# Performance work log

Measured on AMD Instinct MI355X. Metric: run time of the kernel, lower is better.

Reference implementation:

```python
import jax, jax.numpy as jnp
import numpy as np

U = 512  # units

def hard_sigmoid(x):
    # Keras hard_sigmoid: clip(0.2*x + 0.5, 0, 1)
    return jnp.clip(0.2 * x + 0.5, 0.0, 1.0)

def setup_inputs() -> dict:
    key = jax.random.key(0)
    ks = jax.random.split(key, 9)
    B, T, A, D = 64, 2048, 512, 512  # batch, annotation steps, annotation units, input dim
    s = lambda k, shape, scale: jax.random.normal(k, shape, jnp.float32) * scale
    return {
        "inputs": s(ks[0], (B, D), 1.0),
        "h": s(ks[1], (B, U), 1.0),
        "c": s(ks[2], (B, U), 1.0),
        "annotations": s(ks[3], (B, T, A), 1.0),
        "kernel": s(ks[4], (D + A, 4 * U), 0.02),
        "recurrent_kernel": s(ks[5], (U, 4 * U), 0.02),
        "bias": jnp.zeros((6 * U,), jnp.float32).at[U:2 * U].set(1.0),  # unit_forget_bias
        "kernel_u": s(ks[6], (A, U), 0.02),
        "kernel_w": s(ks[7], (U, U), 0.02),
        "kernel_v": s(ks[8], (U,), 0.02),
    }

def reference(inputs, h, c, annotations, kernel, recurrent_kernel, bias, kernel_u, kernel_w, kernel_v):
    bias_u = bias[4 * U:5 * U]
    # precomputed annotation projection (done once in build()): [B,T,U]
    uh = jnp.einsum('bta,au->btu', annotations, kernel_u) + bias_u
    # Bahdanau attention scores
    Wxstm = h @ kernel_w                                   # [B,U]
    et = jnp.einsum('btu,u->bt', jnp.tanh(uh + Wxstm[:, None, :]), kernel_v)
    at = jax.nn.softmax(et, axis=1)                        # exp/sum in source == softmax
    context = jnp.einsum('bt,bta->ba', at, annotations)    # [B,A]
    x = jnp.concatenate([inputs, context], axis=-1)        # [B, D+A]
    z = x @ kernel + h @ recurrent_kernel + bias[:4 * U]   # [B,4U]
    i = hard_sigmoid(z[:, :U])
    f = hard_sigmoid(z[:, U:2 * U])
    c_new = f * c + i * jnp.tanh(z[:, 2 * U:3 * U])
    o = hard_sigmoid(z[:, 3 * U:])
    h_new = o * jnp.tanh(c_new)
    return h_new
```

## Files before the change

### kernel.cpp

```cpp
#include <hip/hip_runtime.h>

constexpr int U = 512;
constexpr int B = 64;
constexpr int T = 2048;
constexpr int A = 512;

typedef __attribute__((ext_vector_type(8))) short short8;
typedef __attribute__((ext_vector_type(4))) float f32x4;

__device__ __forceinline__ unsigned short f32_to_bf16(float f) {
    unsigned int b = __float_as_uint(f);
    unsigned int r = (b + 0x7FFFu + ((b >> 16) & 1u)) >> 16;
    return (unsigned short)r;
}

__device__ __forceinline__ float fast_tanh(float x) {
    float e = exp2f(x * 2.885390081777927f);
    return (e - 1.0f) * __builtin_amdgcn_rcpf(e + 1.0f);
}

__device__ __forceinline__ float hard_sigmoid(float z) {
    return fminf(fmaxf(0.2f * z + 0.5f, 0.0f), 1.0f);
}

__global__ __launch_bounds__(256) void k_prep_s(const float* __restrict__ h,
                                                const float* __restrict__ kw,
                                                float* __restrict__ Sp) {
    int b = blockIdx.x >> 2;
    int kc = blockIdx.x & 3;
    int u = threadIdx.x;
    const float* hb = h + b * U + kc * 128;
    const float* kwb = kw + (size_t)kc * 128 * U;
    float a0 = 0.f, a1 = 0.f;
#pragma unroll 4
    for (int k = 0; k < 128; ++k) {
        float hv = hb[k];
        a0 += hv * kwb[(size_t)k * U + u];
        a1 += hv * kwb[(size_t)k * U + u + 256];
    }
    float* p = Sp + ((size_t)kc * 64 + b) * U;
    p[u] = a0;
    p[u + 256] = a1;
}

__global__ __launch_bounds__(256) void k_s_reduce(const float* __restrict__ Sp,
                                                  const float* __restrict__ bias,
                                                  float* __restrict__ S) {
    int gid = blockIdx.x * 256 + threadIdx.x;
    int b = gid >> 9, u = gid & 511;
    float s = bias[4 * U + u];
#pragma unroll
    for (int kc = 0; kc < 4; ++kc) s += Sp[((size_t)kc * 64 + b) * U + u];
    S[gid] = s;
}

__global__ __launch_bounds__(256) void k_prep_kpack(const float* __restrict__ ku,
                                                    unsigned short* __restrict__ kpack) {
    int t = blockIdx.x >> 3;
    int gid = (blockIdx.x & 7) * 256 + threadIdx.x;
    int d = gid >> 9;
    int u = gid & 511;
    float vals[8];
#pragma unroll
    for (int e = 0; e < 8; ++e) vals[e] = ku[(size_t)(t * 32 + d * 8 + e) * U + u];
    int sc = d ^ ((u >> 1) & 3);
    short8 pk;
#pragma unroll
    for (int e = 0; e < 8; ++e) pk[e] = (short)f32_to_bf16(vals[e]);
    *(short8*)&kpack[(size_t)t * 16384 + u * 32 + sc * 8] = pk;
}

__global__ __launch_bounds__(256) void k_prep_wt(const float* __restrict__ kern,
                                                 const float* __restrict__ rk,
                                                 unsigned short* __restrict__ Wt) {
    __shared__ float tile[32][33];
    int k0 = blockIdx.x << 5;
    int j0 = blockIdx.y << 5;
    int c = threadIdx.x & 31, r0 = threadIdx.x >> 5;
#pragma unroll
    for (int p = 0; p < 4; ++p) {
        int r = r0 + p * 8;
        int k = k0 + r;
        float val = (k < 1024) ? kern[k * 2048 + j0 + c]
                               : rk[(k - 1024) * 2048 + j0 + c];
        tile[r][c] = val;
    }
    __syncthreads();
#pragma unroll
    for (int p = 0; p < 4; ++p) {
        int r = r0 + p * 8;
        Wt[(size_t)(j0 + r) * 1536 + k0 + c] = f32_to_bf16(tile[c][r]);
    }
}

__global__ __launch_bounds__(256, 2) void k_gemm_et(const float* __restrict__ ann,
                                                    const unsigned short* __restrict__ kpack,
                                                    const float* __restrict__ S,
                                                    const float* __restrict__ v,
                                                    float* __restrict__ mz,
                                                    float* __restrict__ part) {
    __shared__ unsigned short As[2][64 * 32];
    __shared__ unsigned short Bs[2][512 * 32];
    __shared__ float red[4][64];
    __shared__ float p_lds[64];

    const int tid = threadIdx.x;
    const int wave = tid >> 6;
    const int lane = tid & 63;
    const int lanelo = lane & 15;
    const int quad = lane >> 4;
    const int wn = wave;

    const int mt = blockIdx.x;
    const int b = mt >> 5;
    const float* aBase = ann + (size_t)mt * 64 * A;
    const char* kpB = (const char*)kpack;

    f32x4 acc[4][8];
#pragma unroll
    for (int i = 0; i < 4; ++i)
#pragma unroll
        for (int j = 0; j < 8; ++j) acc[i][j] = {0.f, 0.f, 0.f, 0.f};

    const int rowA = tid >> 2;
    const int c8A = tid & 3;
    f32x4 pv0, pv1;

    auto stage_b = [&](int t, int buf) {
        const char* src = kpB + (size_t)t * 32768;
#pragma unroll
        for (int p = 0; p < 8; ++p) {
            int seg = p * 4 + wave;
            __builtin_amdgcn_global_load_lds(
                (const __attribute__((address_space(1))) void*)(src + seg * 1024 + lane * 16),
                (__attribute__((address_space(3))) void*)((char*)&Bs[buf][0] + seg * 1024),
                16, 0, 0);
        }
    };

    auto cvt_store = [&](int buf) {
        short8 pk;
        pk[0] = (short)f32_to_bf16(pv0.x);
        pk[1] = (short)f32_to_bf16(pv0.y);
        pk[2] = (short)f32_to_bf16(pv0.z);
        pk[3] = (short)f32_to_bf16(pv0.w);
        pk[4] = (short)f32_to_bf16(pv1.x);
        pk[5] = (short)f32_to_bf16(pv1.y);
        pk[6] = (short)f32_to_bf16(pv1.z);
        pk[7] = (short)f32_to_bf16(pv1.w);
        *(short8*)&As[buf][rowA * 32 + ((c8A ^ ((rowA >> 1) & 3)) * 8)] = pk;
    };

    {
        const float* src = aBase + (size_t)rowA * A + c8A * 8;
        pv0 = *(const f32x4*)src;
        pv1 = *(const f32x4*)(src + 4);
    }
    stage_b(0, 0);
    cvt_store(0);
    __syncthreads();

    for (int t = 0; t < 16; ++t) {
        const int cur = t & 1;
        const int nxt = cur ^ 1;
        const bool more = (t < 15);

        if (more) {
            const float* src = aBase + (size_t)rowA * A + (t + 1) * 32 + c8A * 8;
            pv0 = *(const f32x4*)src;
            pv1 = *(const f32x4*)(src + 4);
            stage_b(t + 1, nxt);
        }

        short8 af[4];
#pragma unroll
        for (int mi = 0; mi < 4; ++mi) {
            int row = mi * 16 + lanelo;
            af[mi] = *(const short8*)&As[cur][row * 32 + ((quad ^ ((row >> 1) & 3)) * 8)];
        }
        short8 bfr[8];
#pragma unroll
        for (int ni = 0; ni < 8; ++ni) {
            int rowb = wn * 128 + ni * 16 + lanelo;
            bfr[ni] = *(const short8*)&Bs[cur][rowb * 32 + ((quad ^ ((rowb >> 1) & 3)) * 8)];
        }
        __builtin_amdgcn_s_setprio(1);
#pragma unroll
        for (int mi = 0; mi < 4; ++mi)
#pragma unroll
            for (int ni = 0; ni < 8; ++ni)
                acc[mi][ni] = __builtin_amdgcn_mfma_f32_16x16x32_bf16(
                    af[mi], bfr[ni], acc[mi][ni], 0, 0, 0);
        __builtin_amdgcn_s_setprio(0);

        if (more) {
            cvt_store(nxt);
        }
        __syncthreads();
    }

    float rows[16];
#pragma unroll
    for (int i = 0; i < 16; ++i) rows[i] = 0.f;
#pragma unroll
    for (int ni = 0; ni < 8; ++ni) {
        int u = wn * 128 + ni * 16 + lanelo;
        float sv = S[b * U + u];
        float vv = v[u];
#pragma unroll
        for (int mi = 0; mi < 4; ++mi)
#pragma unroll
            for (int r = 0; r < 4; ++r)
                rows[mi * 4 + r] += fast_tanh(acc[mi][ni][r] + sv) * vv;
    }
#pragma unroll
    for (int i = 0; i < 16; ++i) {
        rows[i] += __shfl_xor(rows[i], 1);
        rows[i] += __shfl_xor(rows[i], 2);
        rows[i] += __shfl_xor(rows[i], 4);
        rows[i] += __shfl_xor(rows[i], 8);
    }
    if (lanelo == 0) {
#pragma unroll
        for (int mi = 0; mi < 4; ++mi)
#pragma unroll
            for (int r = 0; r < 4; ++r)
                red[wave][mi * 16 + quad * 4 + r] = rows[mi * 4 + r];
    }
    __syncthreads();

    if (tid < 64) {
        float e = red[0][tid] + red[1][tid] + red[2][tid] + red[3][tid];
        float m = e;
#pragma unroll
        for (int o = 1; o < 64; o <<= 1) m = fmaxf(m, __shfl_xor(m, o));
        float p = exp2f((e - m) * 1.4426950408889634f);
        float z = p;
#pragma unroll
        for (int o = 1; o < 64; o <<= 1) z += __shfl_xor(z, o);
        p_lds[tid] = p;
        if (tid == 0) { mz[mt * 2] = m; mz[mt * 2 + 1] = z; }
    }
    __syncthreads();

    float* cbuf = (float*)&Bs[0][0];
    {
        int half = tid >> 7;
        int a4 = (tid & 127) << 2;
        f32x4 cacc = {0.f, 0.f, 0.f, 0.f};
#pragma unroll 4
        for (int t2 = half; t2 < 64; t2 += 2) {
            float w = p_lds[t2];
            f32x4 rv = *(const f32x4*)(aBase + (size_t)t2 * A + a4);
            cacc.x += w * rv.x;
            cacc.y += w * rv.y;
            cacc.z += w * rv.z;
            cacc.w += w * rv.w;
        }
        *(f32x4*)&cbuf[half * 512 + a4] = cacc;
    }
    __syncthreads();
    {
        int a2 = tid << 1;
        float s0 = cbuf[a2] + cbuf[512 + a2];
        float s1 = cbuf[a2 + 1] + cbuf[512 + a2 + 1];
        float* p = part + (size_t)mt * 512;
        p[a2] = s0;
        p[a2 + 1] = s1;
    }
}

__global__ __launch_bounds__(256) void k_ctx_merge_xb(const float* __restrict__ part,
                                                      const float* __restrict__ mz,
                                                      const float* __restrict__ inputs,
                                                      const float* __restrict__ h,
                                                      unsigned short* __restrict__ xb) {
    int b = blockIdx.x;
    int tid = threadIdx.x;
    __shared__ float wsh[32];
    __shared__ float sinvZ;
    if (tid < 32) {
        float m_i = mz[(b * 32 + tid) * 2];
        float z_i = mz[(b * 32 + tid) * 2 + 1];
        float M = m_i;
#pragma unroll
        for (int o = 1; o < 32; o <<= 1) M = fmaxf(M, __shfl_xor(M, o));
        float w = exp2f((m_i - M) * 1.4426950408889634f);
        float wz = w * z_i;
#pragma unroll
        for (int o = 1; o < 32; o <<= 1) wz += __shfl_xor(wz, o);
        wsh[tid] = w;
        if (tid == 0) sinvZ = 1.0f / wz;
    }
    __syncthreads();
    float invZ = sinvZ;
    unsigned short* xrow = xb + (size_t)b * 1536;
#pragma unroll
    for (int i = 0; i < 2; ++i) {
        int a = tid + i * 256;
        float s = 0.f;
#pragma unroll
        for (int c2 = 0; c2 < 32; ++c2)
            s += wsh[c2] * part[((size_t)b * 32 + c2) * 512 + a];
        xrow[512 + a] = f32_to_bf16(s * invZ);
        xrow[a] = f32_to_bf16(inputs[b * 512 + a]);
        xrow[1024 + a] = f32_to_bf16(h[b * 512 + a]);
    }
}

__global__ __launch_bounds__(256) void k_zgemm(const unsigned short* __restrict__ xb,
                                               const unsigned short* __restrict__ Wt,
                                               float* __restrict__ zpart) {
    const int kc = blockIdx.x & 7;
    const int nt = blockIdx.x >> 3;
    const int wave = threadIdx.x >> 6;
    const int lane = threadIdx.x & 63;
    const int lanelo = lane & 15;
    const int quad = lane >> 4;

    const int n = nt * 64 + wave * 16 + lanelo;
    const unsigned short* bp = Wt + (size_t)n * 1536 + kc * 192 + quad * 8;
    const unsigned short* ap = xb + (size_t)lanelo * 1536 + kc * 192 + quad * 8;

    f32x4 acc[4];
#pragma unroll
    for (int i = 0; i < 4; ++i) acc[i] = {0.f, 0.f, 0.f, 0.f};

#pragma unroll
    for (int ks = 0; ks < 6; ++ks) {
        short8 bfrag = *(const short8*)(bp + ks * 32);
#pragma unroll
        for (int mi = 0; mi < 4; ++mi) {
            short8 afrag = *(const short8*)(ap + (size_t)mi * 16 * 1536 + ks * 32);
            acc[mi] = __builtin_amdgcn_mfma_f32_16x16x32_bf16(afrag, bfrag, acc[mi], 0, 0, 0);
        }
    }

    float* p = zpart + (size_t)kc * 64 * 2048;
#pragma unroll
    for (int mi = 0; mi < 4; ++mi)
#pragma unroll
        for (int r = 0; r < 4; ++r) {
            int m = mi * 16 + quad * 4 + r;
            p[(size_t)m * 2048 + n] = acc[mi][r];
        }
}

__global__ __launch_bounds__(256) void k_gates(const float* __restrict__ zpart,
                                               const float* __restrict__ bias,
                                               const float* __restrict__ c,
                                               float* __restrict__ hnew) {
    int gid = blockIdx.x * 256 + threadIdx.x;
    int b = gid >> 9;
    int u = gid & 511;
    float z[4];
#pragma unroll
    for (int g = 0; g < 4; ++g) {
        int j = (g << 9) + u;
        float s = bias[j];
#pragma unroll
        for (int kc = 0; kc < 8; ++kc)
            s += zpart[((size_t)kc * 64 + b) * 2048 + j];
        z[g] = s;
    }
    float ig = hard_sigmoid(z[0]);
    float fg = hard_sigmoid(z[1]);
    float cn = fg * c[b * 512 + u] + ig * fast_tanh(z[2]);
    float og = hard_sigmoid(z[3]);
    hnew[b * 512 + u] = og * fast_tanh(cn);
}

extern "C" void kernel_launch(void* const* d_in, const int* in_sizes, int n_in,
                              void* d_out, int out_size, void* d_ws, size_t ws_size,
                              hipStream_t stream) {
    const float* inputs = (const float*)d_in[0];
    const float* h      = (const float*)d_in[1];
    const float* c      = (const float*)d_in[2];
    const float* ann    = (const float*)d_in[3];
    const float* kern   = (const float*)d_in[4];
    const float* rk     = (const float*)d_in[5];
    const float* bias   = (const float*)d_in[6];
    const float* ku     = (const float*)d_in[7];
    const float* kw     = (const float*)d_in[8];
    const float* kv     = (const float*)d_in[9];

    char* ws = (char*)d_ws;
    float*          S     = (float*)(ws + 0);
    unsigned short* kpack = (unsigned short*)(ws + 131072);
    float*          mz    = (float*)(ws + 655360);
    float*          part  = (float*)(ws + 786432);
    float*          Sp    = (float*)(ws + 4980736);
    unsigned short* xb    = (unsigned short*)(ws + 5505024);
    unsigned short* Wt    = (unsigned short*)(ws + 5701632);
    float*          zpart = (float*)(ws + 11993088);
    float*          hnew  = (float*)d_out;

    k_prep_wt<<<dim3(48, 64), 256, 0, stream>>>(kern, rk, Wt);
    k_prep_kpack<<<128, 256, 0, stream>>>(ku, kpack);
    k_prep_s<<<256, 256, 0, stream>>>(h, kw, Sp);
    k_s_reduce<<<128, 256, 0, stream>>>(Sp, bias, S);
    k_gemm_et<<<2048, 256, 0, stream>>>(ann, kpack, S, kv, mz, part);
    k_ctx_merge_xb<<<64, 256, 0, stream>>>(part, mz, inputs, h, xb);
    k_zgemm<<<256, 256, 0, stream>>>(xb, Wt, zpart);
    k_gates<<<128, 256, 0, stream>>>(zpart, bias, c, hnew);
}
```

Baseline: 484.1 us.

## Enlarge attention GEMM tile to 128 rows with triple-buffered B and manual waitcnt pipelining

The fused attention-score GEMM kernel now handles 128 annotation rows per block using 512 threads (8 waves in a 2x4 layout) instead of 64 rows with 4 waves. Each kpack B tile staged in LDS is therefore reused across twice as many rows. B staging moves to a 3-deep ring buffer with explicit vmcnt/lgkmcnt waits and sched barriers in place of __syncthreads, so global loads overlap the MFMA work. The softmax partials, context reduction and merge kernel are adjusted to 16 chunks per batch. In exchange, LDS use and register pressure per block rise, which may lower occupancy, and the hand-tuned waitcnt counts risk subtle ordering bugs.

Measured after the change: 489.5 us. About the same (+1.1%).

```diff
diff --git a/kernel.cpp b/kernel.cpp
--- a/kernel.cpp
+++ b/kernel.cpp
@@ -22,6 +22,8 @@
 __device__ __forceinline__ float hard_sigmoid(float z) {
     return fminf(fmaxf(0.2f * z + 0.5f, 0.0f), 1.0f);
 }
+
+#define SB() __builtin_amdgcn_sched_barrier(0)
 
 __global__ __launch_bounds__(256) void k_prep_s(const float* __restrict__ h,
                                                 const float* __restrict__ kw,
@@ -93,27 +95,29 @@
     }
 }
 
-__global__ __launch_bounds__(256, 2) void k_gemm_et(const float* __restrict__ ann,
+__global__ __launch_bounds__(512, 2) void k_gemm_et(const float* __restrict__ ann,
                                                     const unsigned short* __restrict__ kpack,
                                                     const float* __restrict__ S,
                                                     const float* __restrict__ v,
                                                     float* __restrict__ mz,
                                                     float* __restrict__ part) {
-    __shared__ unsigned short As[2][64 * 32];
-    __shared__ unsigned short Bs[2][512 * 32];
-    __shared__ float red[4][64];
-    __shared__ float p_lds[64];
+    __shared__ unsigned short As[2][128 * 32];
+    __shared__ unsigned short Bs[3][512 * 32];
+    __shared__ float red[8][64];
+    __shared__ float elds[128];
+    __shared__ float p_lds[128];
 
     const int tid = threadIdx.x;
     const int wave = tid >> 6;
     const int lane = tid & 63;
     const int lanelo = lane & 15;
     const int quad = lane >> 4;
-    const int wn = wave;
+    const int wr = wave >> 2;
+    const int wc = wave & 3;
 
     const int mt = blockIdx.x;
-    const int b = mt >> 5;
-    const float* aBase = ann + (size_t)mt * 64 * A;
+    const int b = mt >> 4;
+    const float* aBase = ann + (size_t)mt * 128 * A;
     const char* kpB = (const char*)kpack;
 
     f32x4 acc[4][8];
@@ -126,18 +130,22 @@
     const int c8A = tid & 3;
     f32x4 pv0, pv1;
 
+    auto load_a = [&](int kk) {
+        const float* src = aBase + (size_t)rowA * A + kk + c8A * 8;
+        pv0 = *(const f32x4*)src;
+        pv1 = *(const f32x4*)(src + 4);
+    };
     auto stage_b = [&](int t, int buf) {
         const char* src = kpB + (size_t)t * 32768;
 #pragma unroll
-        for (int p = 0; p < 8; ++p) {
-            int seg = p * 4 + wave;
+        for (int p = 0; p < 4; ++p) {
+            int seg = p * 8 + wave;
             __builtin_amdgcn_global_load_lds(
                 (const __attribute__((address_space(1))) void*)(src + seg * 1024 + lane * 16),
                 (__attribute__((address_space(3))) void*)((char*)&Bs[buf][0] + seg * 1024),
                 16, 0, 0);
         }
     };
-
     auto cvt_store = [&](int buf) {
         short8 pk;
         pk[0] = (short)f32_to_bf16(pv0.x);
@@ -151,39 +159,46 @@
         *(short8*)&As[buf][rowA * 32 + ((c8A ^ ((rowA >> 1) & 3)) * 8)] = pk;
     };
 
-    {
-        const float* src = aBase + (size_t)rowA * A + c8A * 8;
-        pv0 = *(const f32x4*)src;
-        pv1 = *(const f32x4*)(src + 4);
-    }
+    load_a(0);
+    SB();
     stage_b(0, 0);
+    SB();
+    asm volatile("s_waitcnt vmcnt(4)" ::: "memory");
+    SB();
     cvt_store(0);
-    __syncthreads();
-
+    SB();
+    stage_b(1, 1);
+    SB();
+    asm volatile("s_waitcnt vmcnt(4)" ::: "memory");
+    asm volatile("s_waitcnt lgkmcnt(0)" ::: "memory");
+    __builtin_amdgcn_s_barrier();
+
+#pragma unroll
     for (int t = 0; t < 16; ++t) {
         const int cur = t & 1;
-        const int nxt = cur ^ 1;
-        const bool more = (t < 15);
-
-        if (more) {
-            const float* src = aBase + (size_t)rowA * A + (t + 1) * 32 + c8A * 8;
-            pv0 = *(const f32x4*)src;
-            pv1 = *(const f32x4*)(src + 4);
-            stage_b(t + 1, nxt);
-        }
+        const int curB = t % 3;
+
+        SB();
+        if (t < 15) load_a((t + 1) * 32);
+        SB();
+        if (t < 14) stage_b(t + 2, (t + 2) % 3);
+        SB();
 
         short8 af[4];
 #pragma unroll
         for (int mi = 0; mi < 4; ++mi) {
-            int row = mi * 16 + lanelo;
+            int row = wr * 64 + mi * 16 + lanelo;
             af[mi] = *(const short8*)&As[cur][row * 32 + ((quad ^ ((row >> 1) & 3)) * 8)];
         }
         short8 bfr[8];
 #pragma unroll
         for (int ni = 0; ni < 8; ++ni) {
-            int rowb = wn * 128 + ni * 16 + lanelo;
-            bfr[ni] = *(const short8*)&Bs[cur][rowb * 32 + ((quad ^ ((rowb >> 1) & 3)) * 8)];
-        }
+            int rowb = wc * 128 + ni * 16 + lanelo;
+            bfr[ni] = *(const short8*)&Bs[curB][rowb * 32 + ((quad ^ ((rowb >> 1) & 3)) * 8)];
+        }
+        asm volatile("s_waitcnt lgkmcnt(0)" ::: "memory");
+        SB();
+
         __builtin_amdgcn_s_setprio(1);
 #pragma unroll
         for (int mi = 0; mi < 4; ++mi)
@@ -192,11 +207,16 @@
                 acc[mi][ni] = __builtin_amdgcn_mfma_f32_16x16x32_bf16(
                     af[mi], bfr[ni], acc[mi][ni], 0, 0, 0);
         __builtin_amdgcn_s_setprio(0);
-
-        if (more) {
-            cvt_store(nxt);
-        }
-        __syncthreads();
+        SB();
+
+        if (t < 15) {
+            if (t == 14) { asm volatile("s_waitcnt vmcnt(0)" ::: "memory"); }
+            else         { asm volatile("s_waitcnt vmcnt(4)" ::: "memory"); }
+            SB();
+            cvt_store((t + 1) & 1);
+        }
+        asm volatile("s_waitcnt lgkmcnt(0)" ::: "memory");
+        __builtin_amdgcn_s_barrier();
     }
 
     float rows[16];
@@ -204,7 +224,7 @@
     for (int i = 0; i < 16; ++i) rows[i] = 0.f;
 #pragma unroll
     for (int ni = 0; ni < 8; ++ni) {
-        int u = wn * 128 + ni * 16 + lanelo;
+        int u = wc * 128 + ni * 16 + lanelo;
         float sv = S[b * U + u];
         float vv = v[u];
 #pragma unroll
@@ -229,27 +249,38 @@
     }
     __syncthreads();
 
+    if (tid < 128) {
+        int wrr = tid >> 6;
+        int m = tid & 63;
+        elds[tid] = red[wrr * 4 + 0][m] + red[wrr * 4 + 1][m] +
+                    red[wrr * 4 + 2][m] + red[wrr * 4 + 3][m];
+    }
+    __syncthreads();
+
     if (tid < 64) {
-        float e = red[0][tid] + red[1][tid] + red[2][tid] + red[3][tid];
-        float m = e;
+        float e0 = elds[tid];
+        float e1 = elds[tid + 64];
+        float m = fmaxf(e0, e1);
 #pragma unroll
         for (int o = 1; o < 64; o <<= 1) m = fmaxf(m, __shfl_xor(m, o));
-        float p = exp2f((e - m) * 1.4426950408889634f);
-        float z = p;
+        float p0 = exp2f((e0 - m) * 1.4426950408889634f);
+        float p1 = exp2f((e1 - m) * 1.4426950408889634f);
+        float z = p0 + p1;
 #pragma unroll
         for (int o = 1; o < 64; o <<= 1) z += __shfl_xor(z, o);
-        p_lds[tid] = p;
+        p_lds[tid] = p0;
+        p_lds[tid + 64] = p1;
         if (tid == 0) { mz[mt * 2] = m; mz[mt * 2 + 1] = z; }
     }
     __syncthreads();
 
-    float* cbuf = (float*)&Bs[0][0];
+    float* cbuf = (float*)&As[0][0];
     {
-        int half = tid >> 7;
+        int tg = tid >> 7;
         int a4 = (tid & 127) << 2;
         f32x4 cacc = {0.f, 0.f, 0.f, 0.f};
 #pragma unroll 4
-        for (int t2 = half; t2 < 64; t2 += 2) {
+        for (int t2 = tg; t2 < 128; t2 += 4) {
             float w = p_lds[t2];
             f32x4 rv = *(const f32x4*)(aBase + (size_t)t2 * A + a4);
             cacc.x += w * rv.x;
@@ -257,16 +288,13 @@
             cacc.z += w * rv.z;
             cacc.w += w * rv.w;
         }
-        *(f32x4*)&cbuf[half * 512 + a4] = cacc;
+        *(f32x4*)&cbuf[tg * 512 + a4] = cacc;
     }
     __syncthreads();
     {
-        int a2 = tid << 1;
-        float s0 = cbuf[a2] + cbuf[512 + a2];
-        float s1 = cbuf[a2 + 1] + cbuf[512 + a2 + 1];
-        float* p = part + (size_t)mt * 512;
-        p[a2] = s0;
-        p[a2 + 1] = s1;
+        int a = tid;
+        float s = cbuf[a] + cbuf[512 + a] + cbuf[1024 + a] + cbuf[1536 + a];
+        part[(size_t)mt * 512 + a] = s;
     }
 }
 
@@ -277,18 +305,18 @@
                                                       unsigned short* __restrict__ xb) {
     int b = blockIdx.x;
     int tid = threadIdx.x;
-    __shared__ float wsh[32];
+    __shared__ float wsh[16];
     __shared__ float sinvZ;
-    if (tid < 32) {
-        float m_i = mz[(b * 32 + tid) * 2];
-        float z_i = mz[(b * 32 + tid) * 2 + 1];
+    if (tid < 16) {
+        float m_i = mz[(b * 16 + tid) * 2];
+        float z_i = mz[(b * 16 + tid) * 2 + 1];
         float M = m_i;
 #pragma unroll
-        for (int o = 1; o < 32; o <<= 1) M = fmaxf(M, __shfl_xor(M, o));
+        for (int o = 1; o < 16; o <<= 1) M = fmaxf(M, __shfl_xor(M, o));
         float w = exp2f((m_i - M) * 1.4426950408889634f);
         float wz = w * z_i;
 #pragma unroll
-        for (int o = 1; o < 32; o <<= 1) wz += __shfl_xor(wz, o);
+        for (int o = 1; o < 16; o <<= 1) wz += __shfl_xor(wz, o);
         wsh[tid] = w;
         if (tid == 0) sinvZ = 1.0f / wz;
     }
@@ -300,8 +328,8 @@
         int a = tid + i * 256;
         float s = 0.f;
 #pragma unroll
-        for (int c2 = 0; c2 < 32; ++c2)
-            s += wsh[c2] * part[((size_t)b * 32 + c2) * 512 + a];
+        for (int c2 = 0; c2 < 16; ++c2)
+            s += wsh[c2] * part[((size_t)b * 16 + c2) * 512 + a];
         xrow[512 + a] = f32_to_bf16(s * invZ);
         xrow[a] = f32_to_bf16(inputs[b * 512 + a]);
         xrow[1024 + a] = f32_to_bf16(h[b * 512 + a]);
@@ -388,18 +416,18 @@
     float*          S     = (float*)(ws + 0);
     unsigned short* kpack = (unsigned short*)(ws + 131072);
     float*          mz    = (float*)(ws + 655360);
-    float*          part  = (float*)(ws + 786432);
-    float*          Sp    = (float*)(ws + 4980736);
-    unsigned short* xb    = (unsigned short*)(ws + 5505024);
-    unsigned short* Wt    = (unsigned short*)(ws + 5701632);
-    float*          zpart = (float*)(ws + 11993088);
+    float*          part  = (float*)(ws + 663552);
+    float*          Sp    = (float*)(ws + 2760704);
+    unsigned short* xb    = (unsigned short*)(ws + 3284992);
+    unsigned short* Wt    = (unsigned short*)(ws + 3481600);
+    float*          zpart = (float*)(ws + 9773056);
     float*          hnew  = (float*)d_out;
 
     k_prep_wt<<<dim3(48, 64), 256, 0, stream>>>(kern, rk, Wt);
     k_prep_kpack<<<128, 256, 0, stream>>>(ku, kpack);
     k_prep_s<<<256, 256, 0, stream>>>(h, kw, Sp);
     k_s_reduce<<<128, 256, 0, stream>>>(Sp, bias, S);
-    k_gemm_et<<<2048, 256, 0, stream>>>(ann, kpack, S, kv, mz, part);
+    k_gemm_et<<<1024, 512, 0, stream>>>(ann, kpack, S, kv, mz, part);
     k_ctx_merge_xb<<<64, 256, 0, stream>>>(part, mz, inputs, h, xb);
     k_zgemm<<<256, 256, 0, stream>>>(xb, Wt, zpart);
     k_gates<<<128, 256, 0, stream>>>(zpart, bias, c, hnew);
```
